# Optimization experiments

Measured on AMD Instinct MI355X. Metric: run time of the kernel, lower is better.

## Reference

```python
import jax, jax.numpy as jnp
import numpy as np

N = 50000; E = 800000; F_IN = 128; H = 16; G = 256
DIMS = [F_IN, H, 2 * H, 4 * H, 4 * H, 8 * H]
EPS = 1e-5


def setup_inputs() -> dict:
    key = jax.random.key(0)
    ks = iter(jax.random.split(key, 40))
    inp = {}
    inp["x"] = jax.random.normal(next(ks), (N, F_IN), dtype=jnp.float32)
    inp["edge_index"] = jax.random.randint(next(ks), (2, E), 0, N, dtype=jnp.int32)
    inp["edge_weight"] = jax.random.uniform(next(ks), (E,), dtype=jnp.float32)
    inp["batch"] = jnp.sort(jax.random.randint(next(ks), (N,), 0, G, dtype=jnp.int32))
    for i in range(5):
        din, dout = DIMS[i], DIMS[i + 1]
        inp[f"W{i+1}"] = jax.random.normal(next(ks), (din, dout), dtype=jnp.float32) / np.sqrt(din).astype(np.float32)
        inp[f"b{i+1}"] = jnp.zeros((dout,), jnp.float32)
        inp[f"g{i+1}"] = jnp.ones((dout,), jnp.float32)
        inp[f"bt{i+1}"] = jnp.zeros((dout,), jnp.float32)
    inp["fc1_w"] = jax.random.normal(next(ks), (8 * H, 4 * H), dtype=jnp.float32) / np.sqrt(8 * H).astype(np.float32)
    inp["fc1_b"] = jnp.zeros((4 * H,), jnp.float32)
    inp["fc2_w"] = jax.random.normal(next(ks), (4 * H, 1), dtype=jnp.float32) / np.sqrt(4 * H).astype(np.float32)
    inp["fc2_b"] = jnp.zeros((1,), jnp.float32)
    return inp


def _gcn_norm(edge_index, edge_weight, n):
    # PyG GCNConv: add self-loops (weight 1), symmetric deg^-1/2 normalization.
    loop = jnp.arange(n, dtype=edge_index.dtype)
    row = jnp.concatenate([edge_index[0], loop])  # source
    col = jnp.concatenate([edge_index[1], loop])  # target
    w = jnp.concatenate([edge_weight, jnp.ones((n,), edge_weight.dtype)])
    deg = jax.ops.segment_sum(w, col, num_segments=n)
    dis = jnp.where(deg > 0, jax.lax.rsqrt(jnp.maximum(deg, 1e-12)), 0.0)
    return row, col, dis[row] * w * dis[col]


def _bn(h, g, b):
    # BatchNorm1d, training-mode batch statistics (biased variance, eps=1e-5)
    mu = h.mean(0)
    v = h.var(0)
    return g * (h - mu) * jax.lax.rsqrt(v + EPS) + b


def reference(x, edge_index, edge_weight, batch,
              W1, b1, g1, bt1, W2, b2, g2, bt2, W3, b3, g3, bt3,
              W4, b4, g4, bt4, W5, b5, g5, bt5,
              fc1_w, fc1_b, fc2_w, fc2_b):
    n = x.shape[0]
    row, col, norm = _gcn_norm(edge_index, edge_weight, n)

    def conv(h, W, b):
        m = h @ W                                   # [N, dout] dense transform
        agg = jax.ops.segment_sum(m[row] * norm[:, None], col, num_segments=n)
        return agg + b

    h = _bn(jax.nn.relu(conv(x, W1, b1)), g1, bt1)
    h = _bn(jax.nn.relu(conv(h, W2, b2)), g2, bt2)
    h = _bn(jax.nn.relu(conv(h, W3, b3)), g3, bt3)
    h = jax.nn.relu(_bn(conv(h, W4, b4), g4, bt4))   # layer4: conv->bn->relu
    h = _bn(conv(h, W5, b5), g5, bt5)                # layer5: conv->bn
    pooled = jax.ops.segment_sum(h, batch, num_segments=G)  # global_add_pool -> [G, 8H]
    p = jax.nn.relu(pooled)
    p = jax.nn.relu(p @ fc1_w + fc1_b)
    # dropout is identity in eval mode
    return (p @ fc2_w + fc2_b).reshape(-1)          # [G]
```

## Files before the change

kernel.cpp:

```cpp
#include <hip/hip_runtime.h>

#define NN 50000
#define NE 800000
#define NG 256
#define NBUCKET 16
#define PARTSZ (NBUCKET * 256)

#define NBKT 391
#define ABLK 391
#define ASLICE 2048
#define BCAP 2560

__global__ void k_init(float* part) {
    int i = blockIdx.x * blockDim.x + threadIdx.x;
    if (i < 5 * PARTSZ) part[i] = 0.f;
}

__global__ void kA1(const int* __restrict__ col, int* __restrict__ bb, int e) {
    __shared__ int cnt[NBKT];
    for (int j = threadIdx.x; j < NBKT; j += 256) cnt[j] = 0;
    __syncthreads();
    int start = blockIdx.x * ASLICE;
    int end = min(start + ASLICE, e);
    for (int i = start + threadIdx.x; i < end; i += 256)
        atomicAdd(&cnt[col[i] >> 7], 1);
    __syncthreads();
    for (int j = threadIdx.x; j < NBKT; j += 256) bb[blockIdx.x * NBKT + j] = cnt[j];
}

__global__ void kA2a(int* __restrict__ bb, int* __restrict__ totals) {
    __shared__ int v[ABLK];
    int k = blockIdx.x;
    for (int b = threadIdx.x; b < ABLK; b += 256) v[b] = bb[b * NBKT + k];
    __syncthreads();
    if (threadIdx.x == 0) {
        int run = 0;
        for (int b = 0; b < ABLK; ++b) { int t = v[b]; v[b] = run; run += t; }
        totals[k] = run;
    }
    __syncthreads();
    for (int b = threadIdx.x; b < ABLK; b += 256) bb[b * NBKT + k] = v[b];
}

__global__ void kA2b(const int* __restrict__ totals, int* __restrict__ bucketbase) {
    __shared__ int v[NBKT];
    for (int j = threadIdx.x; j < NBKT; j += 256) v[j] = totals[j];
    __syncthreads();
    if (threadIdx.x == 0) {
        int run = 0;
        for (int k = 0; k < NBKT; ++k) { int t = v[k]; v[k] = run; run += t; }
        bucketbase[NBKT] = run;
    }
    __syncthreads();
    for (int j = threadIdx.x; j < NBKT; j += 256) bucketbase[j] = v[j];
}

__global__ void kA3(const int* __restrict__ row, const int* __restrict__ col,
                    const float* __restrict__ ew, const int* __restrict__ bb,
                    const int* __restrict__ bucketbase, int2* __restrict__ staging, int e) {
    __shared__ int cur[NBKT];
    for (int j = threadIdx.x; j < NBKT; j += 256)
        cur[j] = bucketbase[j] + bb[blockIdx.x * NBKT + j];
    __syncthreads();
    int start = blockIdx.x * ASLICE;
    int end = min(start + ASLICE, e);
    for (int i = start + threadIdx.x; i < end; i += 256) {
        int c = col[i];
        int p = atomicAdd(&cur[c >> 7], 1);
        staging[p] = make_int2(row[i] | ((c & 127) << 16), __float_as_int(ew[i]));
    }
}

__global__ void __launch_bounds__(256) kB(const int* __restrict__ bucketbase,
                                          const int2* __restrict__ staging,
                                          int2* __restrict__ csr, int* __restrict__ ptr,
                                          float* __restrict__ dis, int n) {
    __shared__ int2 st[BCAP];
    __shared__ int2 outb[BCAP];
    __shared__ int hist[129];
    __shared__ int cur[128];
    int k = blockIdx.x, t = threadIdx.x;
    int base = bucketbase[k], cnt = bucketbase[k + 1] - base;
    int node0 = k << 7;
    int ncov = min(128, n - node0);
    if (t < 129) hist[t] = 0;
    __syncthreads();
    if (cnt <= BCAP) {
        for (int i = t; i < cnt; i += 256) {
            int2 v = staging[base + i];
            st[i] = v;
            atomicAdd(&hist[v.x >> 16], 1);
        }
        __syncthreads();
        if (t == 0) {
            int run = 0;
            for (int j = 0; j < 128; ++j) { int h = hist[j]; hist[j] = run; run += h; }
            hist[128] = run;
        }
        __syncthreads();
        if (t < 128) cur[t] = hist[t];
        if (t < ncov) ptr[node0 + t] = base + hist[t];
        __syncthreads();
        for (int i = t; i < cnt; i += 256) {
            int2 v = st[i];
            int j = v.x >> 16;
            int p = atomicAdd(&cur[j], 1);
            outb[p] = make_int2(v.x & 0xFFFF, v.y);
        }
        __syncthreads();
        for (int i = t; i < cnt; i += 256) csr[base + i] = outb[i];
        if (t < ncov) {
            float s = 1.f;
            int a = hist[t], b2 = hist[t + 1];
            for (int p = a; p < b2; ++p) s += __int_as_float(outb[p].y);
            dis[node0 + t] = rsqrtf(s);
        }
    } else {
        for (int i = t; i < cnt; i += 256) atomicAdd(&hist[staging[base + i].x >> 16], 1);
        __syncthreads();
        if (t == 0) {
            int run = 0;
            for (int j = 0; j < 128; ++j) { int h = hist[j]; hist[j] = run; run += h; }
            hist[128] = run;
        }
        __syncthreads();
        if (t < 128) cur[t] = hist[t];
        if (t < ncov) ptr[node0 + t] = base + hist[t];
        __syncthreads();
        for (int i = t; i < cnt; i += 256) {
            int2 v = staging[base + i];
            int j = v.x >> 16;
            int p = atomicAdd(&cur[j], 1);
            csr[base + p] = make_int2(v.x & 0xFFFF, v.y);
        }
        __threadfence_block();
        __syncthreads();
        if (t < ncov) {
            float s = 1.f;
            int a = hist[t], b2 = hist[t + 1];
            for (int p = a; p < b2; ++p) s += __int_as_float(csr[base + p].y);
            dis[node0 + t] = rsqrtf(s);
        }
    }
    if (k == gridDim.x - 1 && t == 0) ptr[n] = bucketbase[NBKT];
}

__global__ void k_scale(const int* __restrict__ ptr, int2* __restrict__ csr,
                        const float* __restrict__ dis, int n) {
    int i = blockIdx.x * blockDim.x + threadIdx.x;
    if (i >= n) return;
    float dc = dis[i];
    int p1 = ptr[i + 1];
    for (int p = ptr[i]; p < p1; ++p) {
        int2 v = csr[p];
        csr[p].y = __float_as_int(dis[v.x] * __int_as_float(v.y) * dc);
    }
}

template <int D, int POSTAFF, int PREAFF, int EPI>
__global__ void k_gather(const float* __restrict__ src, const int* __restrict__ ptr,
                         const int2* __restrict__ csr, const float* __restrict__ dis,
                         const float* __restrict__ partIn, const float* __restrict__ gmv,
                         const float* __restrict__ btv,
                         const float* __restrict__ bias, float* __restrict__ partOut,
                         float* __restrict__ out, int n) {
    const int TPN = D / 4;
    const int CONSUME = POSTAFF || PREAFF;
    __shared__ float ls[EPI ? D : 1], lq[EPI ? D : 1];
    __shared__ float scs[CONSUME ? D : 4], shs[CONSUME ? D : 4];
    int tid = threadIdx.x;
    if (EPI && tid < D) { ls[tid] = 0.f; lq[tid] = 0.f; }
    if (CONSUME && tid < D) {
        float s = 0.f, q = 0.f;
#pragma unroll
        for (int b2 = 0; b2 < NBUCKET; ++b2) {
            s += partIn[b2 * 256 + tid];
            q += partIn[b2 * 256 + 128 + tid];
        }
        float mu = s / (float)n;
        float var = q / (float)n - mu * mu;
        float a = gmv[tid] * rsqrtf(var + 1e-5f);
        scs[tid] = a;
        shs[tid] = btv[tid] - mu * a;
    }
    if (EPI || CONSUME) __syncthreads();

    int t = blockIdx.x * blockDim.x + tid;
    int node = t / TPN;
    int l4 = t - node * TPN;
    bool valid = node < n;
    int nc = valid ? node : n - 1;

    float4 sc = {0,0,0,0}, sh = {0,0,0,0};
    if (CONSUME) {
        sc = ((const float4*)scs)[l4];
        sh = ((const float4*)shs)[l4];
    }
    const float4* s4 = (const float4*)src;
    float d = dis[nc];
    float w0 = d * d;
    float4 v = s4[nc * TPN + l4];
    if (PREAFF) {
        v.x = fmaxf(sc.x * v.x + sh.x, 0.f); v.y = fmaxf(sc.y * v.y + sh.y, 0.f);
        v.z = fmaxf(sc.z * v.z + sh.z, 0.f); v.w = fmaxf(sc.w * v.w + sh.w, 0.f);
    }
    float4 acc = { w0 * v.x, w0 * v.y, w0 * v.z, w0 * v.w };
    float sumw = w0;
    int p0 = ptr[nc], p1 = ptr[nc + 1];
    int p = p0;
    for (; p + 4 <= p1; p += 4) {
        int2 c0 = csr[p], c1 = csr[p+1], c2 = csr[p+2], c3 = csr[p+3];
        float e0 = __int_as_float(c0.y), e1 = __int_as_float(c1.y);
        float e2 = __int_as_float(c2.y), e3 = __int_as_float(c3.y);
        float4 u0 = s4[c0.x * TPN + l4];
        float4 u1 = s4[c1.x * TPN + l4];
        float4 u2 = s4[c2.x * TPN + l4];
        float4 u3 = s4[c3.x * TPN + l4];
        if (PREAFF) {
            u0.x = fmaxf(sc.x*u0.x+sh.x,0.f); u0.y = fmaxf(sc.y*u0.y+sh.y,0.f);
            u0.z = fmaxf(sc.z*u0.z+sh.z,0.f); u0.w = fmaxf(sc.w*u0.w+sh.w,0.f);
            u1.x = fmaxf(sc.x*u1.x+sh.x,0.f); u1.y = fmaxf(sc.y*u1.y+sh.y,0.f);
            u1.z = fmaxf(sc.z*u1.z+sh.z,0.f); u1.w = fmaxf(sc.w*u1.w+sh.w,0.f);
            u2.x = fmaxf(sc.x*u2.x+sh.x,0.f); u2.y = fmaxf(sc.y*u2.y+sh.y,0.f);
            u2.z = fmaxf(sc.z*u2.z+sh.z,0.f); u2.w = fmaxf(sc.w*u2.w+sh.w,0.f);
            u3.x = fmaxf(sc.x*u3.x+sh.x,0.f); u3.y = fmaxf(sc.y*u3.y+sh.y,0.f);
            u3.z = fmaxf(sc.z*u3.z+sh.z,0.f); u3.w = fmaxf(sc.w*u3.w+sh.w,0.f);
        }
        acc.x += e0*u0.x + e1*u1.x + e2*u2.x + e3*u3.x;
        acc.y += e0*u0.y + e1*u1.y + e2*u2.y + e3*u3.y;
        acc.z += e0*u0.z + e1*u1.z + e2*u2.z + e3*u3.z;
        acc.w += e0*u0.w + e1*u1.w + e2*u2.w + e3*u3.w;
        if (POSTAFF) sumw += e0 + e1 + e2 + e3;
    }
    for (; p < p1; ++p) {
        int2 ce = csr[p];
        float w = __int_as_float(ce.y);
        float4 u = s4[ce.x * TPN + l4];
        if (PREAFF) {
            u.x = fmaxf(sc.x*u.x+sh.x,0.f); u.y = fmaxf(sc.y*u.y+sh.y,0.f);
            u.z = fmaxf(sc.z*u.z+sh.z,0.f); u.w = fmaxf(sc.w*u.w+sh.w,0.f);
        }
        acc.x += w*u.x; acc.y += w*u.y; acc.z += w*u.z; acc.w += w*u.w;
        if (POSTAFF) sumw += w;
    }
    if (POSTAFF) {
        acc.x = sc.x * acc.x + sh.x * sumw;
        acc.y = sc.y * acc.y + sh.y * sumw;
        acc.z = sc.z * acc.z + sh.z * sumw;
        acc.w = sc.w * acc.w + sh.w * sumw;
    }
    if (EPI) {
        float4 b = ((const float4*)bias)[l4];
        acc.x = fmaxf(acc.x + b.x, 0.f);
        acc.y = fmaxf(acc.y + b.y, 0.f);
        acc.z = fmaxf(acc.z + b.z, 0.f);
        acc.w = fmaxf(acc.w + b.w, 0.f);
        if (valid) ((float4*)out)[nc * TPN + l4] = acc;
        float s0 = valid ? acc.x : 0.f, s1 = valid ? acc.y : 0.f;
        float s2 = valid ? acc.z : 0.f, s3 = valid ? acc.w : 0.f;
        float q0 = s0*s0, q1 = s1*s1, q2 = s2*s2, q3 = s3*s3;
        for (int off = TPN; off < 64; off <<= 1) {
            s0 += __shfl_down(s0, off, 64); s1 += __shfl_down(s1, off, 64);
            s2 += __shfl_down(s2, off, 64); s3 += __shfl_down(s3, off, 64);
            q0 += __shfl_down(q0, off, 64); q1 += __shfl_down(q1, off, 64);
            q2 += __shfl_down(q2, off, 64); q3 += __shfl_down(q3, off, 64);
        }
        int lane = tid & 63;
        if (lane < TPN) {
            atomicAdd(&ls[4*lane+0], s0); atomicAdd(&ls[4*lane+1], s1);
            atomicAdd(&ls[4*lane+2], s2); atomicAdd(&ls[4*lane+3], s3);
            atomicAdd(&lq[4*lane+0], q0); atomicAdd(&lq[4*lane+1], q1);
            atomicAdd(&lq[4*lane+2], q2); atomicAdd(&lq[4*lane+3], q3);
        }
        __syncthreads();
        int bkt = (blockIdx.x & (NBUCKET - 1)) * 256;
        if (tid < D) {
            atomicAdd(&partOut[bkt + tid], ls[tid]);
            atomicAdd(&partOut[bkt + 128 + tid], lq[tid]);
        }
    } else {
        if (valid) ((float4*)out)[nc * TPN + l4] = acc;
    }
}

template <int DIN, int DOUT, int RELU, int EPI, int NPT>
__global__ void k_gemm(const float* __restrict__ h, const float* __restrict__ W,
                       const float* __restrict__ bias, float* __restrict__ partOut,
                       float* __restrict__ m, int n) {
    const int TPN = DOUT / 4;
    const int GPB = 256 / TPN;
    __shared__ float Wl[DIN * DOUT];
    __shared__ float ls[EPI ? DOUT : 1], lq[EPI ? DOUT : 1];
    int tid = threadIdx.x;
    for (int i = tid; i < DIN * DOUT / 4; i += 256)
        ((float4*)Wl)[i] = ((const float4*)W)[i];
    if (EPI && tid < DOUT) { ls[tid] = 0.f; lq[tid] = 0.f; }
    __syncthreads();

    int jq = tid % TPN;
    int group = tid / TPN;
    int node0 = (blockIdx.x * GPB + group) * NPT;
    const float4* h4 = (const float4*)h;
    int hb[NPT];
    bool val[NPT];
#pragma unroll
    for (int i = 0; i < NPT; ++i) {
        int nd = node0 + i;
        val[i] = nd < n;
        hb[i] = (val[i] ? nd : n - 1) * (DIN / 4);
    }
    float4 acc[NPT];
#pragma unroll
    for (int i = 0; i < NPT; ++i) acc[i] = {0.f, 0.f, 0.f, 0.f};

#pragma unroll 4
    for (int k4 = 0; k4 < DIN / 4; ++k4) {
        const float* wb = &Wl[(k4 * 4) * DOUT + jq * 4];
        float4 w0 = *(const float4*)(wb);
        float4 w1 = *(const float4*)(wb + DOUT);
        float4 w2 = *(const float4*)(wb + 2 * DOUT);
        float4 w3 = *(const float4*)(wb + 3 * DOUT);
#pragma unroll
        for (int i = 0; i < NPT; ++i) {
            float4 hv = h4[hb[i] + k4];
            acc[i].x += hv.x*w0.x + hv.y*w1.x + hv.z*w2.x + hv.w*w3.x;
            acc[i].y += hv.x*w0.y + hv.y*w1.y + hv.z*w2.y + hv.w*w3.y;
            acc[i].z += hv.x*w0.z + hv.y*w1.z + hv.z*w2.z + hv.w*w3.z;
            acc[i].w += hv.x*w0.w + hv.y*w1.w + hv.z*w2.w + hv.w*w3.w;
        }
    }

    float4 bv = {0,0,0,0};
    if (EPI) bv = ((const float4*)bias)[jq];
    float4 sv = {0,0,0,0}, qv = {0,0,0,0};
#pragma unroll
    for (int i = 0; i < NPT; ++i) {
        float4 a = acc[i];
        if (EPI) {
            a.x += bv.x; a.y += bv.y; a.z += bv.z; a.w += bv.w;
            if (RELU) {
                a.x = fmaxf(a.x, 0.f); a.y = fmaxf(a.y, 0.f);
                a.z = fmaxf(a.z, 0.f); a.w = fmaxf(a.w, 0.f);
            }
        }
        if (val[i]) {
            ((float4*)m)[(node0 + i) * TPN + jq] = a;
            if (EPI) {
                sv.x += a.x; sv.y += a.y; sv.z += a.z; sv.w += a.w;
                qv.x += a.x*a.x; qv.y += a.y*a.y; qv.z += a.z*a.z; qv.w += a.w*a.w;
            }
        }
    }
    if (EPI) {
        for (int off = TPN; off < 64; off <<= 1) {
            sv.x += __shfl_down(sv.x, off, 64); sv.y += __shfl_down(sv.y, off, 64);
            sv.z += __shfl_down(sv.z, off, 64); sv.w += __shfl_down(sv.w, off, 64);
            qv.x += __shfl_down(qv.x, off, 64); qv.y += __shfl_down(qv.y, off, 64);
            qv.z += __shfl_down(qv.z, off, 64); qv.w += __shfl_down(qv.w, off, 64);
        }
        int lane = tid & 63;
        if (lane < TPN) {
            atomicAdd(&ls[4*lane+0], sv.x); atomicAdd(&ls[4*lane+1], sv.y);
            atomicAdd(&ls[4*lane+2], sv.z); atomicAdd(&ls[4*lane+3], sv.w);
            atomicAdd(&lq[4*lane+0], qv.x); atomicAdd(&lq[4*lane+1], qv.y);
            atomicAdd(&lq[4*lane+2], qv.z); atomicAdd(&lq[4*lane+3], qv.w);
        }
        __syncthreads();
        int bkt = (blockIdx.x & (NBUCKET - 1)) * 256;
        if (tid < DOUT) {
            atomicAdd(&partOut[bkt + tid], ls[tid]);
            atomicAdd(&partOut[bkt + 128 + tid], lq[tid]);
        }
    }
}

__global__ void k_poolhead(const float* __restrict__ h, const int* __restrict__ batch,
                           const float* __restrict__ partIn, const float* __restrict__ gmv,
                           const float* __restrict__ btv,
                           const float* __restrict__ fc1w, const float* __restrict__ fc1b,
                           const float* __restrict__ fc2w, const float* __restrict__ fc2b,
                           float* __restrict__ out, int n) {
    __shared__ float tmp[256];
    __shared__ float pl[128];
    __shared__ float scs[128], shs[128];
    int g = blockIdx.x;
    int tid = threadIdx.x;
    if (tid < 128) {
        float s = 0.f, q = 0.f;
#pragma unroll
        for (int b2 = 0; b2 < NBUCKET; ++b2) {
            s += partIn[b2 * 256 + tid];
            q += partIn[b2 * 256 + 128 + tid];
        }
        float mu = s / (float)n;
        float var = q / (float)n - mu * mu;
        float a = gmv[tid] * rsqrtf(var + 1e-5f);
        scs[tid] = a;
        shs[tid] = btv[tid] - mu * a;
    }
    int j = tid & 127, prt = tid >> 7;
    int a = 0, b = n;
    while (a < b) { int mid = (a + b) >> 1; if (batch[mid] < g) a = mid + 1; else b = mid; }
    int lo = a;
    b = n;
    while (a < b) { int mid = (a + b) >> 1; if (batch[mid] < g + 1) a = mid + 1; else b = mid; }
    int hi = a;

    float acc = 0.f;
    for (int node = lo + prt; node < hi; node += 2) acc += h[(long)node * 128 + j];
    tmp[tid] = acc;
    __syncthreads();
    if (tid < 128) {
        float cnt = (float)(hi - lo);
        float p = scs[tid] * (tmp[tid] + tmp[tid + 128]) + shs[tid] * cnt;
        pl[tid] = fmaxf(p, 0.f);
    }
    __syncthreads();
    if (tid < 64) {
        float v1 = fc1b[tid];
        for (int k = 0; k < 128; ++k) v1 += pl[k] * fc1w[k * 64 + tid];
        v1 = fmaxf(v1, 0.f);
        float v = v1 * fc2w[tid];
        for (int off = 32; off > 0; off >>= 1) v += __shfl_down(v, off, 64);
        if (tid == 0) out[g] = v + fc2b[0];
    }
}

extern "C" void kernel_launch(void* const* d_in, const int* in_sizes, int n_in,
                              void* d_out, int out_size, void* d_ws, size_t ws_size,
                              hipStream_t stream) {
    const float* x     = (const float*)d_in[0];
    const int*   ei    = (const int*)d_in[1];
    const float* ew    = (const float*)d_in[2];
    const int*   batch = (const int*)d_in[3];
    const float *W[5], *b[5], *gm[5], *bt[5];
    for (int i = 0; i < 5; ++i) {
        W[i]  = (const float*)d_in[4 + 4 * i];
        b[i]  = (const float*)d_in[5 + 4 * i];
        gm[i] = (const float*)d_in[6 + 4 * i];
        bt[i] = (const float*)d_in[7 + 4 * i];
    }
    const float* fc1w = (const float*)d_in[24];
    const float* fc1b = (const float*)d_in[25];
    const float* fc2w = (const float*)d_in[26];
    const float* fc2b = (const float*)d_in[27];
    float* out = (float*)d_out;

    char* wsb = (char*)d_ws;
    float* dis    = (float*)wsb;  wsb += sizeof(float) * NN;
    int*   ptr    = (int*)wsb;    wsb += sizeof(int) * (NN + 4);
    int*   bb     = (int*)wsb;    wsb += sizeof(int) * ABLK * NBKT;
    int*   totals = (int*)wsb;    wsb += sizeof(int) * (NBKT + 1);
    int*   bbase  = (int*)wsb;    wsb += sizeof(int) * (NBKT + 3);
    int2*  staging= (int2*)wsb;   wsb += sizeof(int2) * NE;
    int2*  csr    = (int2*)wsb;   wsb += sizeof(int2) * NE;
    float* part   = (float*)wsb;  wsb += sizeof(float) * 5 * PARTSZ;
    float* buf1   = (float*)wsb;  wsb += sizeof(float) * (long)NN * 128;
    float* buf2   = (float*)wsb;  wsb += sizeof(float) * (long)NN * 128;

    const int* row = ei;
    const int* col = ei + NE;
    const int B = 256;
    const int NB_N = (NN + B - 1) / B;

    k_init<<<(5 * PARTSZ + B - 1) / B, B, 0, stream>>>(part);
    kA1<<<ABLK, B, 0, stream>>>(col, bb, NE);
    kA2a<<<NBKT, B, 0, stream>>>(bb, totals);
    kA2b<<<1, B, 0, stream>>>(totals, bbase);
    kA3<<<ABLK, B, 0, stream>>>(row, col, ew, bb, bbase, staging, NE);
    kB<<<NBKT, B, 0, stream>>>(bbase, staging, csr, ptr, dis, NN);
    k_scale<<<NB_N, B, 0, stream>>>(ptr, csr, dis, NN);

    auto grid4 = [](long threads) { return (int)((threads + 255) / 256); };
    auto ggrid = [](int npb) { return (NN + npb - 1) / npb; };

    k_gemm<128, 16, 0, 0, 2><<<ggrid((256/4)*2), B, 0, stream>>>(x, W[0], b[0], nullptr, buf1, NN);
    k_gather<16, 0, 0, 1><<<grid4((long)NN * 4), B, 0, stream>>>(buf1, ptr, csr, dis,
                                                                 nullptr, nullptr, nullptr,
                                                                 b[0], part + 0 * PARTSZ, buf2, NN);

    k_gather<16, 1, 0, 0><<<grid4((long)NN * 4), B, 0, stream>>>(buf2, ptr, csr, dis,
                                                                 part + 0 * PARTSZ, gm[0], bt[0],
                                                                 nullptr, nullptr, buf1, NN);
    k_gemm<16, 32, 1, 1, 4><<<ggrid((256/8)*4), B, 0, stream>>>(buf1, W[1], b[1], part + 1 * PARTSZ, buf2, NN);

    k_gather<32, 1, 0, 0><<<grid4((long)NN * 8), B, 0, stream>>>(buf2, ptr, csr, dis,
                                                                 part + 1 * PARTSZ, gm[1], bt[1],
                                                                 nullptr, nullptr, buf1, NN);
    k_gemm<32, 64, 1, 1, 4><<<ggrid((256/16)*4), B, 0, stream>>>(buf1, W[2], b[2], part + 2 * PARTSZ, buf2, NN);

    k_gather<64, 1, 0, 0><<<grid4((long)NN * 16), B, 0, stream>>>(buf2, ptr, csr, dis,
                                                                  part + 2 * PARTSZ, gm[2], bt[2],
                                                                  nullptr, nullptr, buf1, NN);
    k_gemm<64, 64, 0, 1, 4><<<ggrid((256/16)*4), B, 0, stream>>>(buf1, W[3], b[3], part + 3 * PARTSZ, buf2, NN);

    k_gather<64, 0, 1, 0><<<grid4((long)NN * 16), B, 0, stream>>>(buf2, ptr, csr, dis,
                                                                  part + 3 * PARTSZ, gm[3], bt[3],
                                                                  nullptr, nullptr, buf1, NN);
    k_gemm<64, 128, 0, 1, 4><<<ggrid((256/32)*4), B, 0, stream>>>(buf1, W[4], b[4], part + 4 * PARTSZ, buf2, NN);

    k_poolhead<<<NG, 256, 0, stream>>>(buf2, batch, part + 4 * PARTSZ, gm[4], bt[4],
                                       fc1w, fc1b, fc2w, fc2b, out, NN);
}
```

Baseline: 440.7 us.

## Split each node's edge list across lanes in gather and fuse edge scaling into first GEMM

The gather kernel gains an EP parameter so that for the wider layers (D=32, 64) each node's incoming edges are split across 4 lane groups and the partial sums are combined with xor shuffles. This raises the memory-level parallelism of the irregular neighbor gather. Separately, the standalone edge-normalization scaling kernel is folded into extra blocks of the first GEMM launch, removing one launch and letting the two run concurrently. The costs are more threads, shuffle reductions, and idle lane groups for nodes with few edges.

```diff
diff --git a/kernel.cpp b/kernel.cpp
--- a/kernel.cpp
+++ b/kernel.cpp
@@ -145,19 +145,7 @@
     if (k == gridDim.x - 1 && t == 0) ptr[n] = bucketbase[NBKT];
 }
 
-__global__ void k_scale(const int* __restrict__ ptr, int2* __restrict__ csr,
-                        const float* __restrict__ dis, int n) {
-    int i = blockIdx.x * blockDim.x + threadIdx.x;
-    if (i >= n) return;
-    float dc = dis[i];
-    int p1 = ptr[i + 1];
-    for (int p = ptr[i]; p < p1; ++p) {
-        int2 v = csr[p];
-        csr[p].y = __float_as_int(dis[v.x] * __int_as_float(v.y) * dc);
-    }
-}
-
-template <int D, int POSTAFF, int PREAFF, int EPI>
+template <int D, int EP, int POSTAFF, int PREAFF, int EPI>
 __global__ void k_gather(const float* __restrict__ src, const int* __restrict__ ptr,
                          const int2* __restrict__ csr, const float* __restrict__ dis,
                          const float* __restrict__ partIn, const float* __restrict__ gmv,
@@ -165,6 +153,7 @@
                          const float* __restrict__ bias, float* __restrict__ partOut,
                          float* __restrict__ out, int n) {
     const int TPN = D / 4;
+    const int LPN = TPN * EP;
     const int CONSUME = POSTAFF || PREAFF;
     __shared__ float ls[EPI ? D : 1], lq[EPI ? D : 1];
     __shared__ float scs[CONSUME ? D : 4], shs[CONSUME ? D : 4];
@@ -186,8 +175,10 @@
     if (EPI || CONSUME) __syncthreads();
 
     int t = blockIdx.x * blockDim.x + tid;
-    int node = t / TPN;
-    int l4 = t - node * TPN;
+    int node = t / LPN;
+    int r = t - node * LPN;
+    int e0 = r / TPN;
+    int l4 = r - e0 * TPN;
     bool valid = node < n;
     int nc = valid ? node : n - 1;
 
@@ -197,21 +188,25 @@
         sh = ((const float4*)shs)[l4];
     }
     const float4* s4 = (const float4*)src;
-    float d = dis[nc];
-    float w0 = d * d;
-    float4 v = s4[nc * TPN + l4];
-    if (PREAFF) {
-        v.x = fmaxf(sc.x * v.x + sh.x, 0.f); v.y = fmaxf(sc.y * v.y + sh.y, 0.f);
-        v.z = fmaxf(sc.z * v.z + sh.z, 0.f); v.w = fmaxf(sc.w * v.w + sh.w, 0.f);
-    }
-    float4 acc = { w0 * v.x, w0 * v.y, w0 * v.z, w0 * v.w };
-    float sumw = w0;
+    float4 acc = {0.f, 0.f, 0.f, 0.f};
+    float sumw = 0.f;
+    if (e0 == 0) {
+        float d = dis[nc];
+        float w0 = d * d;
+        float4 v = s4[nc * TPN + l4];
+        if (PREAFF) {
+            v.x = fmaxf(sc.x * v.x + sh.x, 0.f); v.y = fmaxf(sc.y * v.y + sh.y, 0.f);
+            v.z = fmaxf(sc.z * v.z + sh.z, 0.f); v.w = fmaxf(sc.w * v.w + sh.w, 0.f);
+        }
+        acc.x = w0 * v.x; acc.y = w0 * v.y; acc.z = w0 * v.z; acc.w = w0 * v.w;
+        sumw = w0;
+    }
     int p0 = ptr[nc], p1 = ptr[nc + 1];
-    int p = p0;
-    for (; p + 4 <= p1; p += 4) {
-        int2 c0 = csr[p], c1 = csr[p+1], c2 = csr[p+2], c3 = csr[p+3];
-        float e0 = __int_as_float(c0.y), e1 = __int_as_float(c1.y);
-        float e2 = __int_as_float(c2.y), e3 = __int_as_float(c3.y);
+    int p = p0 + e0;
+    for (; p + 3 * EP < p1; p += 4 * EP) {
+        int2 c0 = csr[p], c1 = csr[p + EP], c2 = csr[p + 2 * EP], c3 = csr[p + 3 * EP];
+        float e0w = __int_as_float(c0.y), e1w = __int_as_float(c1.y);
+        float e2w = __int_as_float(c2.y), e3w = __int_as_float(c3.y);
         float4 u0 = s4[c0.x * TPN + l4];
         float4 u1 = s4[c1.x * TPN + l4];
         float4 u2 = s4[c2.x * TPN + l4];
@@ -226,13 +221,13 @@
             u3.x = fmaxf(sc.x*u3.x+sh.x,0.f); u3.y = fmaxf(sc.y*u3.y+sh.y,0.f);
             u3.z = fmaxf(sc.z*u3.z+sh.z,0.f); u3.w = fmaxf(sc.w*u3.w+sh.w,0.f);
         }
-        acc.x += e0*u0.x + e1*u1.x + e2*u2.x + e3*u3.x;
-        acc.y += e0*u0.y + e1*u1.y + e2*u2.y + e3*u3.y;
-        acc.z += e0*u0.z + e1*u1.z + e2*u2.z + e3*u3.z;
-        acc.w += e0*u0.w + e1*u1.w + e2*u2.w + e3*u3.w;
-        if (POSTAFF) sumw += e0 + e1 + e2 + e3;
-    }
-    for (; p < p1; ++p) {
+        acc.x += e0w*u0.x + e1w*u1.x + e2w*u2.x + e3w*u3.x;
+        acc.y += e0w*u0.y + e1w*u1.y + e2w*u2.y + e3w*u3.y;
+        acc.z += e0w*u0.z + e1w*u1.z + e2w*u2.z + e3w*u3.z;
+        acc.w += e0w*u0.w + e1w*u1.w + e2w*u2.w + e3w*u3.w;
+        if (POSTAFF) sumw += e0w + e1w + e2w + e3w;
+    }
+    for (; p < p1; p += EP) {
         int2 ce = csr[p];
         float w = __int_as_float(ce.y);
         float4 u = s4[ce.x * TPN + l4];
@@ -242,6 +237,16 @@
         }
         acc.x += w*u.x; acc.y += w*u.y; acc.z += w*u.z; acc.w += w*u.w;
         if (POSTAFF) sumw += w;
+    }
+    if (EP > 1) {
+#pragma unroll
+        for (int off = TPN; off < LPN; off <<= 1) {
+            acc.x += __shfl_xor(acc.x, off, 64);
+            acc.y += __shfl_xor(acc.y, off, 64);
+            acc.z += __shfl_xor(acc.z, off, 64);
+            acc.w += __shfl_xor(acc.w, off, 64);
+            if (POSTAFF) sumw += __shfl_xor(sumw, off, 64);
+        }
     }
     if (POSTAFF) {
         acc.x = sc.x * acc.x + sh.x * sumw;
@@ -279,14 +284,28 @@
             atomicAdd(&partOut[bkt + 128 + tid], lq[tid]);
         }
     } else {
-        if (valid) ((float4*)out)[nc * TPN + l4] = acc;
-    }
-}
-
-template <int DIN, int DOUT, int RELU, int EPI, int NPT>
+        if (valid && e0 == 0) ((float4*)out)[nc * TPN + l4] = acc;
+    }
+}
+
+template <int DIN, int DOUT, int RELU, int EPI, int NPT, int SCALE>
 __global__ void k_gemm(const float* __restrict__ h, const float* __restrict__ W,
                        const float* __restrict__ bias, float* __restrict__ partOut,
-                       float* __restrict__ m, int n) {
+                       float* __restrict__ m, int n,
+                       const int* __restrict__ ptr, int2* __restrict__ csr,
+                       const float* __restrict__ dis, int gemmBlocks) {
+    if (SCALE && (int)blockIdx.x >= gemmBlocks) {
+        int i = ((int)blockIdx.x - gemmBlocks) * 256 + threadIdx.x;
+        if (i < n) {
+            float dc = dis[i];
+            int pp1 = ptr[i + 1];
+            for (int p = ptr[i]; p < pp1; ++p) {
+                int2 v = csr[p];
+                csr[p].y = __float_as_int(dis[v.x] * __int_as_float(v.y) * dc);
+            }
+        }
+        return;
+    }
     const int TPN = DOUT / 4;
     const int GPB = 256 / TPN;
     __shared__ float Wl[DIN * DOUT];
@@ -469,35 +488,42 @@
     kA2b<<<1, B, 0, stream>>>(totals, bbase);
     kA3<<<ABLK, B, 0, stream>>>(row, col, ew, bb, bbase, staging, NE);
     kB<<<NBKT, B, 0, stream>>>(bbase, staging, csr, ptr, dis, NN);
-    k_scale<<<NB_N, B, 0, stream>>>(ptr, csr, dis, NN);
 
     auto grid4 = [](long threads) { return (int)((threads + 255) / 256); };
     auto ggrid = [](int npb) { return (NN + npb - 1) / npb; };
 
-    k_gemm<128, 16, 0, 0, 2><<<ggrid((256/4)*2), B, 0, stream>>>(x, W[0], b[0], nullptr, buf1, NN);
-    k_gather<16, 0, 0, 1><<<grid4((long)NN * 4), B, 0, stream>>>(buf1, ptr, csr, dis,
-                                                                 nullptr, nullptr, nullptr,
-                                                                 b[0], part + 0 * PARTSZ, buf2, NN);
-
-    k_gather<16, 1, 0, 0><<<grid4((long)NN * 4), B, 0, stream>>>(buf2, ptr, csr, dis,
-                                                                 part + 0 * PARTSZ, gm[0], bt[0],
-                                                                 nullptr, nullptr, buf1, NN);
-    k_gemm<16, 32, 1, 1, 4><<<ggrid((256/8)*4), B, 0, stream>>>(buf1, W[1], b[1], part + 1 * PARTSZ, buf2, NN);
-
-    k_gather<32, 1, 0, 0><<<grid4((long)NN * 8), B, 0, stream>>>(buf2, ptr, csr, dis,
-                                                                 part + 1 * PARTSZ, gm[1], bt[1],
-                                                                 nullptr, nullptr, buf1, NN);
-    k_gemm<32, 64, 1, 1, 4><<<ggrid((256/16)*4), B, 0, stream>>>(buf1, W[2], b[2], part + 2 * PARTSZ, buf2, NN);
-
-    k_gather<64, 1, 0, 0><<<grid4((long)NN * 16), B, 0, stream>>>(buf2, ptr, csr, dis,
-                                                                  part + 2 * PARTSZ, gm[2], bt[2],
-                                                                  nullptr, nullptr, buf1, NN);
-    k_gemm<64, 64, 0, 1, 4><<<ggrid((256/16)*4), B, 0, stream>>>(buf1, W[3], b[3], part + 3 * PARTSZ, buf2, NN);
-
-    k_gather<64, 0, 1, 0><<<grid4((long)NN * 16), B, 0, stream>>>(buf2, ptr, csr, dis,
-                                                                  part + 3 * PARTSZ, gm[3], bt[3],
-                                                                  nullptr, nullptr, buf1, NN);
-    k_gemm<64, 128, 0, 1, 4><<<ggrid((256/32)*4), B, 0, stream>>>(buf1, W[4], b[4], part + 4 * PARTSZ, buf2, NN);
+    {
+        int gemmBlocks = ggrid((256 / 4) * 2);
+        k_gemm<128, 16, 0, 0, 2, 1><<<gemmBlocks + NB_N, B, 0, stream>>>(
+            x, W[0], b[0], nullptr, buf1, NN, ptr, csr, dis, gemmBlocks);
+    }
+    k_gather<16, 1, 0, 0, 1><<<grid4((long)NN * 4), B, 0, stream>>>(buf1, ptr, csr, dis,
+                                                                    nullptr, nullptr, nullptr,
+                                                                    b[0], part + 0 * PARTSZ, buf2, NN);
+
+    k_gather<16, 1, 1, 0, 0><<<grid4((long)NN * 4), B, 0, stream>>>(buf2, ptr, csr, dis,
+                                                                    part + 0 * PARTSZ, gm[0], bt[0],
+                                                                    nullptr, nullptr, buf1, NN);
+    k_gemm<16, 32, 1, 1, 4, 0><<<ggrid((256/8)*4), B, 0, stream>>>(buf1, W[1], b[1], part + 1 * PARTSZ,
+                                                                   buf2, NN, nullptr, nullptr, nullptr, 0);
+
+    k_gather<32, 4, 1, 0, 0><<<grid4((long)NN * 32), B, 0, stream>>>(buf2, ptr, csr, dis,
+                                                                     part + 1 * PARTSZ, gm[1], bt[1],
+                                                                     nullptr, nullptr, buf1, NN);
+    k_gemm<32, 64, 1, 1, 4, 0><<<ggrid((256/16)*4), B, 0, stream>>>(buf1, W[2], b[2], part + 2 * PARTSZ,
+                                                                    buf2, NN, nullptr, nullptr, nullptr, 0);
+
+    k_gather<64, 4, 1, 0, 0><<<grid4((long)NN * 64), B, 0, stream>>>(buf2, ptr, csr, dis,
+                                                                     part + 2 * PARTSZ, gm[2], bt[2],
+                                                                     nullptr, nullptr, buf1, NN);
+    k_gemm<64, 64, 0, 1, 4, 0><<<ggrid((256/16)*4), B, 0, stream>>>(buf1, W[3], b[3], part + 3 * PARTSZ,
+                                                                    buf2, NN, nullptr, nullptr, nullptr, 0);
+
+    k_gather<64, 4, 0, 1, 0><<<grid4((long)NN * 64), B, 0, stream>>>(buf2, ptr, csr, dis,
+                                                                     part + 3 * PARTSZ, gm[3], bt[3],
+                                                                     nullptr, nullptr, buf1, NN);
+    k_gemm<64, 128, 0, 1, 4, 0><<<ggrid((256/32)*4), B, 0, stream>>>(buf1, W[4], b[4], part + 4 * PARTSZ,
+                                                                     buf2, NN, nullptr, nullptr, nullptr, 0);
 
     k_poolhead<<<NG, 256, 0, stream>>>(buf2, batch, part + 4 * PARTSZ, gm[4], bt[4],
                                        fc1w, fc1b, fc2w, fc2b, out, NN);
```

Result: slower. 465.7 us (+5.7%).
